# Kernel optimization log

Measured on AMD Instinct MI355X. Metric: run time of the kernel, lower is better.

Reference implementation:

```python
import jax, jax.numpy as jnp
import numpy as np

EPS_LN = 1e-5
EPS_ACT = 1e-5
EPS_W = 1e-8


def _layer_norm(x):
    # F.layer_norm(x, [d]) with no affine params, eps=1e-5, biased variance
    mu = jnp.mean(x, axis=-1, keepdims=True)
    xc = x - mu
    var = jnp.mean(xc * xc, axis=-1, keepdims=True)
    return xc * jax.lax.rsqrt(var + EPS_LN)


def _activation_quant(x):
    # per-token absmax int8 fake-quant (dequantized back to float)
    scale = 127.0 / jnp.clip(jnp.max(jnp.abs(x), axis=-1, keepdims=True), EPS_ACT)
    return jnp.clip(jnp.round(x * scale), -128, 127) / scale


def _weight_quant(w):
    # ternary {-1,0,+1} absmean quantization, rescaled by absmean
    scale = jnp.clip(jnp.mean(jnp.abs(w)), EPS_W)
    return jnp.clip(jnp.round(w / scale), -1, 1) * scale


def _bitlinear(x, w, b):
    xn = _layer_norm(x)
    xq = _activation_quant(xn)        # forward value (STE irrelevant for fwd)
    wq = _weight_quant(w)
    return jnp.einsum('bsd,fd->bsf', xq, wq) + b


def setup_inputs() -> dict:
    key = jax.random.key(0)
    k1, k2, k3, k4, k5 = jax.random.split(key, 5)
    d_model, d_ff = 2048, 8192
    B, S = 4, 2048
    x = jax.random.normal(k1, (B, S, d_model), dtype=jnp.float32)
    # nn.Linear default init: U(-1/sqrt(fan_in), 1/sqrt(fan_in))
    lim1 = 1.0 / np.sqrt(d_model)
    lim2 = 1.0 / np.sqrt(d_ff)
    w1 = jax.random.uniform(k2, (d_ff, d_model), jnp.float32, -lim1, lim1)
    b1 = jax.random.uniform(k3, (d_ff,), jnp.float32, -lim1, lim1)
    w2 = jax.random.uniform(k4, (d_model, d_ff), jnp.float32, -lim2, lim2)
    b2 = jax.random.uniform(k5, (d_model,), jnp.float32, -lim2, lim2)
    return {"x": x, "w1": w1, "b1": b1, "w2": w2, "b2": b2}


def reference(x, w1, b1, w2, b2):
    h = _bitlinear(x, w1, b1)
    h = jax.nn.gelu(h, approximate=False)  # torch F.gelu default = exact erf
    # dropout p=0.0 -> identity
    return _bitlinear(h, w2, b2)
```

## Files before the change

kernel.cpp:

```cpp
#include <hip/hip_runtime.h>

typedef int     i32x4 __attribute__((ext_vector_type(4)));
typedef _Float16 f16x2 __attribute__((ext_vector_type(2)));

__device__ __forceinline__ void async_cp16(const void* g, void* l) {
    __builtin_amdgcn_global_load_lds(
        (const __attribute__((address_space(1))) void*)g,
        (__attribute__((address_space(3))) void*)l, 16, 0, 0);
}

template <bool GELU, typename OutT>
__global__ __launch_bounds__(256) void gemm_i8(
    const signed char* __restrict__ A,
    const signed char* __restrict__ B,
    const float* __restrict__ rowinv,
    const float* __restrict__ wscale,
    const float* __restrict__ bias,
    OutT* __restrict__ C,
    int M, int N, int K)
{
    __shared__ signed char sA[128 * 128];
    __shared__ signed char sB[128 * 128];

    const int tid  = threadIdx.x;
    const int lane = tid & 63;
    const int wid  = tid >> 6;
    const int lm   = lane & 15;
    const int quad = lane >> 4;
    const int wr   = (wid >> 1) * 64;
    const int wc   = (wid & 1) * 64;

    const long long rowA0 = (long long)blockIdx.y * 128;
    const long long rowB0 = (long long)blockIdx.x * 128;

    const int srow   = tid >> 3;
    const int slot   = tid & 7;
    const int gchunk = slot ^ (srow & 7);

    const signed char* aP = A + (rowA0 + srow) * (long long)K + gchunk * 16;
    const signed char* bP = B + (rowB0 + srow) * (long long)K + gchunk * 16;
    signed char* sA_t = &sA[tid * 16];
    signed char* sB_t = &sB[tid * 16];
    const long long rstep = 32LL * K;

    i32x4 acc[4][4] = {};

    const int swz = lm & 7;

    for (int k0 = 0; k0 < K; k0 += 128) {
#pragma unroll
        for (int r = 0; r < 4; ++r) {
            async_cp16(aP + r * rstep + k0, sA_t + r * 4096);
            async_cp16(bP + r * rstep + k0, sB_t + r * 4096);
        }
        __syncthreads();
#pragma unroll
        for (int ks = 0; ks < 2; ++ks) {
            const int coff = ((ks * 4 + quad) ^ swz) * 16;
            i32x4 af[4], bfr[4];
#pragma unroll
            for (int i = 0; i < 4; ++i)
                af[i] = *(const i32x4*)&sA[(wr + i * 16 + lm) * 128 + coff];
#pragma unroll
            for (int j = 0; j < 4; ++j)
                bfr[j] = *(const i32x4*)&sB[(wc + j * 16 + lm) * 128 + coff];
#pragma unroll
            for (int i = 0; i < 4; ++i)
#pragma unroll
                for (int j = 0; j < 4; ++j)
                    acc[i][j] = __builtin_amdgcn_mfma_i32_16x16x64_i8(
                        af[i], bfr[j], acc[i][j], 0, 0, 0);
        }
        __syncthreads();
    }

    const float sw = wscale[0];
    float bj[4];
#pragma unroll
    for (int j = 0; j < 4; ++j)
        bj[j] = bias[rowB0 + wc + j * 16 + lm];

#pragma unroll
    for (int i = 0; i < 4; ++i) {
#pragma unroll
        for (int r = 0; r < 4; ++r) {
            const long long gr = rowA0 + wr + i * 16 + quad * 4 + r;
            const float rs = sw * rowinv[gr];
#pragma unroll
            for (int j = 0; j < 4; ++j) {
                const long long gc = rowB0 + wc + j * 16 + lm;
                float v = (float)acc[i][j][r] * rs + bj[j];
                if constexpr (GELU)
                    v = 0.5f * v * (1.0f + erff(v * 0.70710678118654752f));
                C[gr * (long long)N + gc] = (OutT)v;
            }
        }
    }
}

__global__ __launch_bounds__(256) void ln_quant_x(
    const float* __restrict__ x, signed char* __restrict__ xq,
    float* __restrict__ xinv)
{
    const int t = blockIdx.x;
    const int tid = threadIdx.x;
    const int lane = tid & 63, wid = tid >> 6;
    const float4* row = (const float4*)(x + (long long)t * 2048);
    float4 v0 = row[tid];
    float4 v1 = row[tid + 256];
    float vv[8] = {v0.x, v0.y, v0.z, v0.w, v1.x, v1.y, v1.z, v1.w};

    float s = 0.f, mn = vv[0], mx = vv[0];
#pragma unroll
    for (int i = 0; i < 8; ++i) { s += vv[i]; mn = fminf(mn, vv[i]); mx = fmaxf(mx, vv[i]); }
#pragma unroll
    for (int off = 32; off > 0; off >>= 1) {
        s += __shfl_down(s, off);
        mn = fminf(mn, __shfl_down(mn, off));
        mx = fmaxf(mx, __shfl_down(mx, off));
    }
    __shared__ float rS[4], rMn[4], rMx[4];
    if (lane == 0) { rS[wid] = s; rMn[wid] = mn; rMx[wid] = mx; }
    __syncthreads();
    s  = rS[0] + rS[1] + rS[2] + rS[3];
    mn = fminf(fminf(rMn[0], rMn[1]), fminf(rMn[2], rMn[3]));
    mx = fmaxf(fmaxf(rMx[0], rMx[1]), fmaxf(rMx[2], rMx[3]));
    const float mu = s * (1.0f / 2048.0f);

    float ssc = 0.f;
#pragma unroll
    for (int i = 0; i < 8; ++i) { float d = vv[i] - mu; ssc += d * d; }
#pragma unroll
    for (int off = 32; off > 0; off >>= 1) ssc += __shfl_down(ssc, off);
    __syncthreads();
    if (lane == 0) rS[wid] = ssc;
    __syncthreads();
    ssc = rS[0] + rS[1] + rS[2] + rS[3];

    const float var  = ssc * (1.0f / 2048.0f);
    const float rstd = 1.0f / sqrtf(var + 1e-5f);
    float am = fmaxf(mx - mu, mu - mn) * rstd;
    am = fmaxf(am, 1e-5f);
    const float scale = 127.0f / am;

    unsigned int b0 = 0, b1 = 0;
#pragma unroll
    for (int i = 0; i < 8; ++i) {
        float xn = (vv[i] - mu) * rstd;
        int qi = (int)fminf(fmaxf(rintf(xn * scale), -128.0f), 127.0f);
        unsigned int byte = (unsigned int)(qi & 0xff);
        if (i < 4) b0 |= byte << (i * 8);
        else       b1 |= byte << ((i - 4) * 8);
    }
    int* orow = (int*)(xq + (long long)t * 2048);
    orow[tid]       = (int)b0;
    orow[tid + 256] = (int)b1;
    if (tid == 0) xinv[t] = am / 127.0f;
}

__global__ __launch_bounds__(256) void ln_quant_h(
    const unsigned short* __restrict__ h, signed char* __restrict__ hq,
    float* __restrict__ hinv)
{
    const long long t = blockIdx.x;
    const int tid = threadIdx.x;
    const int lane = tid & 63, wid = tid >> 6;
    const unsigned short* row = h + t * 8192;

    uint4 raw[4];
    float v[32];
#pragma unroll
    for (int c = 0; c < 4; ++c) raw[c] = ((const uint4*)row)[c * 256 + tid];
#pragma unroll
    for (int c = 0; c < 4; ++c) {
        unsigned int u[4] = {raw[c].x, raw[c].y, raw[c].z, raw[c].w};
#pragma unroll
        for (int k = 0; k < 4; ++k) {
            f16x2 p = __builtin_bit_cast(f16x2, u[k]);
            v[c * 8 + k * 2 + 0] = (float)p[0];
            v[c * 8 + k * 2 + 1] = (float)p[1];
        }
    }

    float s = 0.f, mn = v[0], mx = v[0];
#pragma unroll
    for (int i = 0; i < 32; ++i) { s += v[i]; mn = fminf(mn, v[i]); mx = fmaxf(mx, v[i]); }
#pragma unroll
    for (int off = 32; off > 0; off >>= 1) {
        s += __shfl_down(s, off);
        mn = fminf(mn, __shfl_down(mn, off));
        mx = fmaxf(mx, __shfl_down(mx, off));
    }
    __shared__ float rS[4], rMn[4], rMx[4];
    if (lane == 0) { rS[wid] = s; rMn[wid] = mn; rMx[wid] = mx; }
    __syncthreads();
    s  = rS[0] + rS[1] + rS[2] + rS[3];
    mn = fminf(fminf(rMn[0], rMn[1]), fminf(rMn[2], rMn[3]));
    mx = fmaxf(fmaxf(rMx[0], rMx[1]), fmaxf(rMx[2], rMx[3]));
    const float mu = s * (1.0f / 8192.0f);

    float ssc = 0.f;
#pragma unroll
    for (int i = 0; i < 32; ++i) { float d = v[i] - mu; ssc += d * d; }
#pragma unroll
    for (int off = 32; off > 0; off >>= 1) ssc += __shfl_down(ssc, off);
    __syncthreads();
    if (lane == 0) rS[wid] = ssc;
    __syncthreads();
    ssc = rS[0] + rS[1] + rS[2] + rS[3];

    const float var  = ssc * (1.0f / 8192.0f);
    const float rstd = 1.0f / sqrtf(var + 1e-5f);
    float am = fmaxf(mx - mu, mu - mn) * rstd;
    am = fmaxf(am, 1e-5f);
    const float scale = 127.0f / am;

    signed char* orow = hq + t * 8192;
#pragma unroll
    for (int c = 0; c < 4; ++c) {
        unsigned int b0 = 0, b1 = 0;
#pragma unroll
        for (int k = 0; k < 8; ++k) {
            float xn = (v[c * 8 + k] - mu) * rstd;
            int qi = (int)fminf(fmaxf(rintf(xn * scale), -128.0f), 127.0f);
            unsigned int byte = (unsigned int)(qi & 0xff);
            if (k < 4) b0 |= byte << (k * 8);
            else       b1 |= byte << ((k - 4) * 8);
        }
        int2 o; o.x = (int)b0; o.y = (int)b1;
        ((int2*)orow)[c * 256 + tid] = o;
    }
    if (tid == 0) hinv[t] = am / 127.0f;
}

__global__ __launch_bounds__(256) void reduce_abs(
    const float4* __restrict__ w4, int n4, float* __restrict__ partial)
{
    const int tid = threadIdx.x;
    const int lane = tid & 63, wid = tid >> 6;
    float s = 0.f;
    for (int i = blockIdx.x * 256 + tid; i < n4; i += gridDim.x * 256) {
        float4 v = w4[i];
        s += fabsf(v.x) + fabsf(v.y) + fabsf(v.z) + fabsf(v.w);
    }
#pragma unroll
    for (int off = 32; off > 0; off >>= 1) s += __shfl_down(s, off);
    __shared__ float rS[4];
    if (lane == 0) rS[wid] = s;
    __syncthreads();
    if (tid == 0) partial[blockIdx.x] = rS[0] + rS[1] + rS[2] + rS[3];
}

__global__ __launch_bounds__(256) void finalize_scales(
    const float* __restrict__ p1, const float* __restrict__ p2,
    float* __restrict__ scales)
{
    const int tid = threadIdx.x;
    const int lane = tid & 63, wid = tid >> 6;
    float s1 = 0.f, s2 = 0.f;
    for (int i = tid; i < 1024; i += 256) { s1 += p1[i]; s2 += p2[i]; }
#pragma unroll
    for (int off = 32; off > 0; off >>= 1) {
        s1 += __shfl_down(s1, off);
        s2 += __shfl_down(s2, off);
    }
    __shared__ float rA[4], rB[4];
    if (lane == 0) { rA[wid] = s1; rB[wid] = s2; }
    __syncthreads();
    if (tid == 0) {
        float m1 = fmaxf((rA[0] + rA[1] + rA[2] + rA[3]) * (1.0f / 16777216.0f), 1e-8f);
        float m2 = fmaxf((rB[0] + rB[1] + rB[2] + rB[3]) * (1.0f / 16777216.0f), 1e-8f);
        scales[0] = m1;
        scales[1] = m2;
    }
}

__global__ __launch_bounds__(256) void quant_w(
    const float4* __restrict__ w4, signed char* __restrict__ wq,
    const float* __restrict__ scales, int sidx, int n4)
{
    const float s = scales[sidx];
    for (int i = blockIdx.x * 256 + threadIdx.x; i < n4; i += gridDim.x * 256) {
        float4 v = w4[i];
        int q0 = (int)fminf(fmaxf(rintf(v.x / s), -1.0f), 1.0f);
        int q1 = (int)fminf(fmaxf(rintf(v.y / s), -1.0f), 1.0f);
        int q2 = (int)fminf(fmaxf(rintf(v.z / s), -1.0f), 1.0f);
        int q3 = (int)fminf(fmaxf(rintf(v.w / s), -1.0f), 1.0f);
        unsigned int p = (unsigned int)(q0 & 0xff) | ((unsigned int)(q1 & 0xff) << 8)
                       | ((unsigned int)(q2 & 0xff) << 16) | ((unsigned int)(q3 & 0xff) << 24);
        ((unsigned int*)wq)[i] = p;
    }
}

extern "C" void kernel_launch(void* const* d_in, const int* in_sizes, int n_in,
                              void* d_out, int out_size, void* d_ws, size_t ws_size,
                              hipStream_t stream)
{
    const float* x  = (const float*)d_in[0];
    const float* w1 = (const float*)d_in[1];
    const float* b1 = (const float*)d_in[2];
    const float* w2 = (const float*)d_in[3];
    const float* b2 = (const float*)d_in[4];
    float* out = (float*)d_out;

    char* ws = (char*)d_ws;
    const size_t SZ_WQ = 16777216;
    signed char* w1q = (signed char*)(ws);
    signed char* w2q = (signed char*)(ws + SZ_WQ);
    signed char* xq  = (signed char*)(ws + 2 * SZ_WQ);
    unsigned short* h = (unsigned short*)(ws + 3 * SZ_WQ);
    signed char* hq  = (signed char*)(ws + 3 * SZ_WQ + 134217728);
    float* xinv   = (float*)(ws + 3 * SZ_WQ + 134217728 + 67108864);
    float* hinv   = xinv + 8192;
    float* part1  = hinv + 8192;
    float* part2  = part1 + 1024;
    float* scales = part2 + 1024;

    const int N4W = 4194304;

    reduce_abs<<<1024, 256, 0, stream>>>((const float4*)w1, N4W, part1);
    reduce_abs<<<1024, 256, 0, stream>>>((const float4*)w2, N4W, part2);
    finalize_scales<<<1, 256, 0, stream>>>(part1, part2, scales);
    quant_w<<<4096, 256, 0, stream>>>((const float4*)w1, w1q, scales, 0, N4W);
    quant_w<<<4096, 256, 0, stream>>>((const float4*)w2, w2q, scales, 1, N4W);
    ln_quant_x<<<8192, 256, 0, stream>>>(x, xq, xinv);

    gemm_i8<true, _Float16><<<dim3(64, 64), 256, 0, stream>>>(
        xq, w1q, xinv, &scales[0], b1, (_Float16*)h, 8192, 8192, 2048);

    ln_quant_h<<<8192, 256, 0, stream>>>(h, hq, hinv);

    gemm_i8<false, float><<<dim3(16, 64), 256, 0, stream>>>(
        hq, w2q, hinv, &scales[1], b2, out, 8192, 2048, 8192);
}
```

Baseline: 629.7 us.

## Switch int8 GEMM to 32x32x32 MFMA with 2-wave blocks; merge weight-prep launches

The int8 GEMM moves from 16x16x64 MFMA with 4 waves per 128x128 tile to 32x32x32 MFMA with 2 waves. Each wave now computes a 128x64 sub-tile, which raises register blocking and reduces LDS fragment reads per MFMA. The tile loader is adjusted so 128 threads still fill the 128x128 LDS tiles. Separately, the two weight reductions and the two weight quantizations are each merged into a single launch covering both matrices, cutting launch overhead. The trade-off is fewer waves per block, so latency hiding may drop, and accumulator register pressure goes up.

```diff
diff --git a/kernel.cpp b/kernel.cpp
--- a/kernel.cpp
+++ b/kernel.cpp
@@ -1,7 +1,8 @@
 #include <hip/hip_runtime.h>
 
-typedef int     i32x4 __attribute__((ext_vector_type(4)));
-typedef _Float16 f16x2 __attribute__((ext_vector_type(2)));
+typedef int      i32x4  __attribute__((ext_vector_type(4)));
+typedef int      i32x16 __attribute__((ext_vector_type(16)));
+typedef _Float16 f16x2  __attribute__((ext_vector_type(2)));
 
 __device__ __forceinline__ void async_cp16(const void* g, void* l) {
     __builtin_amdgcn_global_load_lds(
@@ -10,7 +11,7 @@
 }
 
 template <bool GELU, typename OutT>
-__global__ __launch_bounds__(256) void gemm_i8(
+__global__ __launch_bounds__(128) void gemm_i8(
     const signed char* __restrict__ A,
     const signed char* __restrict__ B,
     const float* __restrict__ rowinv,
@@ -25,10 +26,9 @@
     const int tid  = threadIdx.x;
     const int lane = tid & 63;
     const int wid  = tid >> 6;
-    const int lm   = lane & 15;
-    const int quad = lane >> 4;
-    const int wr   = (wid >> 1) * 64;
-    const int wc   = (wid & 1) * 64;
+    const int l32  = lane & 31;
+    const int h    = lane >> 5;
+    const int wc   = wid * 64;
 
     const long long rowA0 = (long long)blockIdx.y * 128;
     const long long rowB0 = (long long)blockIdx.x * 128;
@@ -41,55 +41,56 @@
     const signed char* bP = B + (rowB0 + srow) * (long long)K + gchunk * 16;
     signed char* sA_t = &sA[tid * 16];
     signed char* sB_t = &sB[tid * 16];
-    const long long rstep = 32LL * K;
-
-    i32x4 acc[4][4] = {};
-
-    const int swz = lm & 7;
+    const long long rstep = 16LL * K;
+
+    i32x16 acc[4][2] = {};
+
+    const int swz = lane & 7;
 
     for (int k0 = 0; k0 < K; k0 += 128) {
 #pragma unroll
-        for (int r = 0; r < 4; ++r) {
-            async_cp16(aP + r * rstep + k0, sA_t + r * 4096);
-            async_cp16(bP + r * rstep + k0, sB_t + r * 4096);
+        for (int r = 0; r < 8; ++r) {
+            async_cp16(aP + r * rstep + k0, sA_t + r * 2048);
+            async_cp16(bP + r * rstep + k0, sB_t + r * 2048);
         }
         __syncthreads();
 #pragma unroll
-        for (int ks = 0; ks < 2; ++ks) {
-            const int coff = ((ks * 4 + quad) ^ swz) * 16;
-            i32x4 af[4], bfr[4];
+        for (int ks = 0; ks < 4; ++ks) {
+            const int coff = ((ks * 2 + h) ^ swz) * 16;
+            i32x4 af[4], bfr[2];
 #pragma unroll
             for (int i = 0; i < 4; ++i)
-                af[i] = *(const i32x4*)&sA[(wr + i * 16 + lm) * 128 + coff];
-#pragma unroll
-            for (int j = 0; j < 4; ++j)
-                bfr[j] = *(const i32x4*)&sB[(wc + j * 16 + lm) * 128 + coff];
+                af[i] = *(const i32x4*)&sA[(i * 32 + l32) * 128 + coff];
+#pragma unroll
+            for (int j = 0; j < 2; ++j)
+                bfr[j] = *(const i32x4*)&sB[(wc + j * 32 + l32) * 128 + coff];
 #pragma unroll
             for (int i = 0; i < 4; ++i)
 #pragma unroll
-                for (int j = 0; j < 4; ++j)
-                    acc[i][j] = __builtin_amdgcn_mfma_i32_16x16x64_i8(
+                for (int j = 0; j < 2; ++j)
+                    acc[i][j] = __builtin_amdgcn_mfma_i32_32x32x32_i8(
                         af[i], bfr[j], acc[i][j], 0, 0, 0);
         }
         __syncthreads();
     }
 
     const float sw = wscale[0];
-    float bj[4];
-#pragma unroll
-    for (int j = 0; j < 4; ++j)
-        bj[j] = bias[rowB0 + wc + j * 16 + lm];
+    float bj[2];
+#pragma unroll
+    for (int j = 0; j < 2; ++j)
+        bj[j] = bias[rowB0 + wc + j * 32 + l32];
 
 #pragma unroll
     for (int i = 0; i < 4; ++i) {
 #pragma unroll
-        for (int r = 0; r < 4; ++r) {
-            const long long gr = rowA0 + wr + i * 16 + quad * 4 + r;
+        for (int reg = 0; reg < 16; ++reg) {
+            const int rowt = (reg & 3) + 8 * (reg >> 2) + 4 * h;
+            const long long gr = rowA0 + i * 32 + rowt;
             const float rs = sw * rowinv[gr];
 #pragma unroll
-            for (int j = 0; j < 4; ++j) {
-                const long long gc = rowB0 + wc + j * 16 + lm;
-                float v = (float)acc[i][j][r] * rs + bj[j];
+            for (int j = 0; j < 2; ++j) {
+                const long long gc = rowB0 + wc + j * 32 + l32;
+                float v = (float)acc[i][j][reg] * rs + bj[j];
                 if constexpr (GELU)
                     v = 0.5f * v * (1.0f + erff(v * 0.70710678118654752f));
                 C[gr * (long long)N + gc] = (OutT)v;
@@ -233,13 +234,17 @@
     if (tid == 0) hinv[t] = am / 127.0f;
 }
 
-__global__ __launch_bounds__(256) void reduce_abs(
-    const float4* __restrict__ w4, int n4, float* __restrict__ partial)
+__global__ __launch_bounds__(256) void reduce_abs2(
+    const float4* __restrict__ w1, const float4* __restrict__ w2,
+    int n4, float* __restrict__ partial)
 {
     const int tid = threadIdx.x;
     const int lane = tid & 63, wid = tid >> 6;
+    const int half = blockIdx.x >> 10;
+    const int b    = blockIdx.x & 1023;
+    const float4* w4 = half ? w2 : w1;
     float s = 0.f;
-    for (int i = blockIdx.x * 256 + tid; i < n4; i += gridDim.x * 256) {
+    for (int i = b * 256 + tid; i < n4; i += 1024 * 256) {
         float4 v = w4[i];
         s += fabsf(v.x) + fabsf(v.y) + fabsf(v.z) + fabsf(v.w);
     }
@@ -275,12 +280,17 @@
     }
 }
 
-__global__ __launch_bounds__(256) void quant_w(
-    const float4* __restrict__ w4, signed char* __restrict__ wq,
-    const float* __restrict__ scales, int sidx, int n4)
-{
-    const float s = scales[sidx];
-    for (int i = blockIdx.x * 256 + threadIdx.x; i < n4; i += gridDim.x * 256) {
+__global__ __launch_bounds__(256) void quant_w2k(
+    const float4* __restrict__ w1, const float4* __restrict__ w2,
+    signed char* __restrict__ w1q, signed char* __restrict__ w2q,
+    const float* __restrict__ scales, int n4)
+{
+    const int half = blockIdx.x >> 12;
+    const int b    = blockIdx.x & 4095;
+    const float4* w4 = half ? w2 : w1;
+    signed char* wq  = half ? w2q : w1q;
+    const float s = scales[half];
+    for (int i = b * 256 + threadIdx.x; i < n4; i += 4096 * 256) {
         float4 v = w4[i];
         int q0 = (int)fminf(fmaxf(rintf(v.x / s), -1.0f), 1.0f);
         int q1 = (int)fminf(fmaxf(rintf(v.y / s), -1.0f), 1.0f);
@@ -312,24 +322,22 @@
     signed char* hq  = (signed char*)(ws + 3 * SZ_WQ + 134217728);
     float* xinv   = (float*)(ws + 3 * SZ_WQ + 134217728 + 67108864);
     float* hinv   = xinv + 8192;
-    float* part1  = hinv + 8192;
-    float* part2  = part1 + 1024;
-    float* scales = part2 + 1024;
+    float* part   = hinv + 8192;
+    float* scales = part + 2048;
 
     const int N4W = 4194304;
 
-    reduce_abs<<<1024, 256, 0, stream>>>((const float4*)w1, N4W, part1);
-    reduce_abs<<<1024, 256, 0, stream>>>((const float4*)w2, N4W, part2);
-    finalize_scales<<<1, 256, 0, stream>>>(part1, part2, scales);
-    quant_w<<<4096, 256, 0, stream>>>((const float4*)w1, w1q, scales, 0, N4W);
-    quant_w<<<4096, 256, 0, stream>>>((const float4*)w2, w2q, scales, 1, N4W);
+    reduce_abs2<<<2048, 256, 0, stream>>>((const float4*)w1, (const float4*)w2, N4W, part);
+    finalize_scales<<<1, 256, 0, stream>>>(part, part + 1024, scales);
+    quant_w2k<<<8192, 256, 0, stream>>>((const float4*)w1, (const float4*)w2,
+                                        w1q, w2q, scales, N4W);
     ln_quant_x<<<8192, 256, 0, stream>>>(x, xq, xinv);
 
-    gemm_i8<true, _Float16><<<dim3(64, 64), 256, 0, stream>>>(
+    gemm_i8<true, _Float16><<<dim3(64, 64), 128, 0, stream>>>(
         xq, w1q, xinv, &scales[0], b1, (_Float16*)h, 8192, 8192, 2048);
 
     ln_quant_h<<<8192, 256, 0, stream>>>(h, hq, hinv);
 
-    gemm_i8<false, float><<<dim3(16, 64), 256, 0, stream>>>(
+    gemm_i8<false, float><<<dim3(16, 64), 128, 0, stream>>>(
         hq, w2q, hinv, &scales[1], b2, out, 8192, 2048, 8192);
 }
```

After: 757.4 us. 1.2x slower.
